# Optimization experiments

Hardware: AMD Instinct MI355X
Metric: run time of the kernel (lower is better)

The kernel has to match this reference:

```python
import jax, jax.numpy as jnp
import numpy as np

N = 20000      # nodes
E = 320000     # edges (every node has >=1 incoming edge)
IN = 512       # input feature dim
HID = 128      # per-head hidden dim
H = 8          # heads
C = 64         # classes (final layer hidden dim)
SLOPE = 0.01   # torch F.leaky_relu default negative_slope


def _gat_head(x, src, dst, W, b, al, alb, ar, arb):
    # x: [N, D_in]; W: [D_in, D_h]; al/ar: [D_h]; alb/arb: scalar
    ft = x @ W + b                       # [N, D_h]
    a1 = ft @ al + alb                   # [N] dst-side logit
    a2 = ft @ ar + arb                   # [N] src-side logit
    s = jax.nn.leaky_relu(a1[dst] + a2[src], SLOPE)   # [E]
    smax = jax.ops.segment_max(s, dst, num_segments=N)
    e = jnp.exp(s - smax[dst])
    denom = jax.ops.segment_sum(e, dst, num_segments=N)
    w = e / denom[dst]                   # segment softmax over incoming edges
    accum = jax.ops.segment_sum(w[:, None] * ft[src], dst, num_segments=N)
    return jax.nn.elu(accum)             # GATFinalize (no residual)


def setup_inputs() -> dict:
    key = jax.random.key(0)
    ks = jax.random.split(key, 16)

    def lin(k, i, o):
        return (jax.random.normal(k, (i, o), jnp.float32) / np.sqrt(i))

    features = jax.random.normal(ks[0], (N, IN), jnp.float32)
    src = jax.random.randint(ks[1], (E,), 0, N, jnp.int32)
    dst = jnp.concatenate([
        jnp.arange(N, dtype=jnp.int32),
        jax.random.randint(ks[2], (E - N,), 0, N, jnp.int32),
    ])

    # layer 0: H heads, in_dim -> HID
    W0 = jax.random.normal(ks[3], (H, IN, HID), jnp.float32) / np.sqrt(IN)
    b0 = jnp.zeros((H, HID), jnp.float32)
    al0 = jax.random.normal(ks[4], (H, HID), jnp.float32) / np.sqrt(HID)
    alb0 = jnp.zeros((H,), jnp.float32)
    ar0 = jax.random.normal(ks[5], (H, HID), jnp.float32) / np.sqrt(HID)
    arb0 = jnp.zeros((H,), jnp.float32)

    # layer 1: H heads, H*HID -> HID
    W1 = jax.random.normal(ks[6], (H, H * HID, HID), jnp.float32) / np.sqrt(H * HID)
    b1 = jnp.zeros((H, HID), jnp.float32)
    al1 = jax.random.normal(ks[7], (H, HID), jnp.float32) / np.sqrt(HID)
    alb1 = jnp.zeros((H,), jnp.float32)
    ar1 = jax.random.normal(ks[8], (H, HID), jnp.float32) / np.sqrt(HID)
    arb1 = jnp.zeros((H,), jnp.float32)

    # final: single head, H*HID -> C
    Wf = lin(ks[9], H * HID, C)
    bf = jnp.zeros((C,), jnp.float32)
    alf = jax.random.normal(ks[10], (C,), jnp.float32) / np.sqrt(C)
    albf = jnp.zeros((), jnp.float32)
    arf = jax.random.normal(ks[11], (C,), jnp.float32) / np.sqrt(C)
    arbf = jnp.zeros((), jnp.float32)

    return dict(features=features, src=src, dst=dst,
                W0=W0, b0=b0, al0=al0, alb0=alb0, ar0=ar0, arb0=arb0,
                W1=W1, b1=b1, al1=al1, alb1=alb1, ar1=ar1, arb1=arb1,
                Wf=Wf, bf=bf, alf=alf, albf=albf, arf=arf, arbf=arbf)


def reference(features, src, dst,
              W0, b0, al0, alb0, ar0, arb0,
              W1, b1, al1, alb1, ar1, arb1,
              Wf, bf, alf, albf, arf, arbf):
    x = features
    # layer 0: concat heads -> [N, H*HID]
    x = jnp.concatenate([
        _gat_head(x, src, dst, W0[h], b0[h], al0[h], alb0[h], ar0[h], arb0[h])
        for h in range(H)], axis=1)
    # layer 1
    x = jnp.concatenate([
        _gat_head(x, src, dst, W1[h], b1[h], al1[h], alb1[h], ar1[h], arb1[h])
        for h in range(H)], axis=1)
    # final single-head output layer -> [N, C]
    return _gat_head(x, src, dst, Wf, bf, alf, albf, arf, arbf)
```

## Files before the change

### kernel.cpp

```cpp
#include <hip/hip_runtime.h>
#include <math.h>

#define N_NODES 20000
#define N_EDGES 320000
#define D_IN    512
#define D_HID   128
#define N_HEADS 8
#define N_CLS   64

typedef __bf16 bf16x8 __attribute__((ext_vector_type(8)));
typedef float  f32x4  __attribute__((ext_vector_type(4)));

__device__ __forceinline__ float leaky(float x) { return fmaxf(x, 0.01f * x); }

__device__ __forceinline__ unsigned short f2bf(float f) {
    unsigned u = __float_as_uint(f);
    return (unsigned short)((u + 0x7FFFu + ((u >> 16) & 1u)) >> 16);
}
__device__ __forceinline__ float bflo(unsigned v) { return __uint_as_float(v << 16); }
__device__ __forceinline__ float bfhi(unsigned v) { return __uint_as_float(v & 0xffff0000u); }

__device__ __forceinline__ void gl_lds16(const void* g, void* l) {
    __builtin_amdgcn_global_load_lds((const __attribute__((address_space(1))) void*)g,
                                     (__attribute__((address_space(3))) void*)l, 16, 0, 0);
}

__global__ void k_zero(int* __restrict__ p, int n) {
    int i = blockIdx.x * blockDim.x + threadIdx.x;
    if (i < n) p[i] = 0;
}

__global__ void k_count(const int* __restrict__ dst, int* __restrict__ counts, int e) {
    int i = blockIdx.x * blockDim.x + threadIdx.x;
    if (i < e) atomicAdd(&counts[dst[i]], 1);
}

__global__ void k_scan(const int* __restrict__ counts, int* __restrict__ indptr,
                       int* __restrict__ cursor, int n) {
    __shared__ int sdata[1024];
    __shared__ int srun;
    int t = threadIdx.x;
    if (t == 0) srun = 0;
    __syncthreads();
    for (int base = 0; base < n; base += 1024) {
        int idx = base + t;
        int v = (idx < n) ? counts[idx] : 0;
        sdata[t] = v;
        __syncthreads();
        for (int off = 1; off < 1024; off <<= 1) {
            int x = (t >= off) ? sdata[t - off] : 0;
            __syncthreads();
            sdata[t] += x;
            __syncthreads();
        }
        int incl = sdata[t];
        int run = srun;
        if (idx < n) {
            indptr[idx] = run + incl - v;
            cursor[idx] = run + incl - v;
        }
        __syncthreads();
        if (t == 1023) srun = run + incl;
        __syncthreads();
    }
    if (t == 0) indptr[n] = srun;
}

__global__ void k_scatter(const int* __restrict__ src, const int* __restrict__ dst,
                          int* __restrict__ cursor, int* __restrict__ csr_src, int e) {
    int i = blockIdx.x * blockDim.x + threadIdx.x;
    if (i < e) {
        int pos = atomicAdd(&cursor[dst[i]], 1);
        csr_src[pos] = src[i];
    }
}

__global__ void k_cvtA(const float* __restrict__ in, unsigned short* __restrict__ out, int n4) {
    int i = blockIdx.x * blockDim.x + threadIdx.x;
    if (i < n4) {
        float4 v = ((const float4*)in)[i];
        unsigned long long pk =
            (unsigned long long)f2bf(v.x) | ((unsigned long long)f2bf(v.y) << 16) |
            ((unsigned long long)f2bf(v.z) << 32) | ((unsigned long long)f2bf(v.w) << 48);
        *(unsigned long long*)(out + (size_t)i * 4) = pk;
    }
}

__global__ void k_cvtW(const float* __restrict__ W, unsigned short* __restrict__ Wt,
                       int K, int Nf) {
    __shared__ float t[64][65];
    int k0 = blockIdx.x * 64, n0 = blockIdx.y * 64, h = blockIdx.z;
    const float* Wh = W + (size_t)h * K * Nf;
    unsigned short* Wth = Wt + (size_t)h * K * Nf;
    int tx = threadIdx.x & 63, ty = threadIdx.x >> 6;
#pragma unroll
    for (int i = 0; i < 16; ++i) {
        int k = ty + i * 4;
        t[k][tx] = Wh[(size_t)(k0 + k) * Nf + n0 + tx];
    }
    __syncthreads();
#pragma unroll
    for (int i = 0; i < 16; ++i) {
        int n = ty + i * 4;
        Wth[(size_t)(n0 + n) * K + k0 + tx] = f2bf(t[tx][n]);
    }
}

__global__ __launch_bounds__(256) void k_gemm_fused(
    const unsigned short* __restrict__ A, const unsigned short* __restrict__ Bt,
    const float* __restrict__ bias, const float* __restrict__ al,
    const float* __restrict__ alb, const float* __restrict__ ar,
    const float* __restrict__ arb, unsigned short* __restrict__ C,
    float* __restrict__ a1, float* __restrict__ a2, int M, int K)
{
    constexpr int BM = 128, BK = 64, BNP = 256;
    __shared__ unsigned short As[BM * BK];
    __shared__ unsigned short Bs[BNP * BK];

    const int tid  = threadIdx.x;
    const int lane = tid & 63;
    const int wid  = tid >> 6;
    const int wm   = wid >> 1;
    const int wn   = wid & 1;
    const int m0   = blockIdx.x * BM;
    const int h0   = blockIdx.z * 2;
    const int h    = h0 + wn;

    const unsigned short* Bth = Bt + (size_t)h0 * 128 * K;
    const int rsub = lane & 15;
    const int rhi  = lane >> 4;
    const int wbase = tid & ~63;

    f32x4 acc[4][8];
#pragma unroll
    for (int i = 0; i < 4; ++i)
#pragma unroll
        for (int j = 0; j < 8; ++j) acc[i][j] = (f32x4){0.f, 0.f, 0.f, 0.f};

    for (int k0 = 0; k0 < K; k0 += BK) {
#pragma unroll
        for (int p = 0; p < 4; ++p) {
            int o    = (p * 256 + tid) * 16;
            int row  = o >> 7;
            int icol = (o & 127) ^ ((row & 7) << 4);
            int grow = m0 + row; if (grow > M - 1) grow = M - 1;
            gl_lds16(A + (size_t)grow * K + k0 + (icol >> 1),
                     (void*)((char*)As + (p * 256 + wbase) * 16));
        }
#pragma unroll
        for (int p = 0; p < 8; ++p) {
            int o    = (p * 256 + tid) * 16;
            int row  = o >> 7;
            int icol = (o & 127) ^ ((row & 7) << 4);
            gl_lds16(Bth + (size_t)row * K + k0 + (icol >> 1),
                     (void*)((char*)Bs + (p * 256 + wbase) * 16));
        }
        __syncthreads();

#pragma unroll
        for (int q = 0; q < 2; ++q) {
            bf16x8 av[4], bv[8];
#pragma unroll
            for (int mi = 0; mi < 4; ++mi) {
                int row  = wm * 64 + mi * 16 + rsub;
                int icol = (q * 64 + rhi * 16) ^ ((row & 7) << 4);
                av[mi] = *(const bf16x8*)((const char*)As + row * 128 + icol);
            }
#pragma unroll
            for (int ni = 0; ni < 8; ++ni) {
                int row  = wn * 128 + ni * 16 + rsub;
                int icol = (q * 64 + rhi * 16) ^ ((row & 7) << 4);
                bv[ni] = *(const bf16x8*)((const char*)Bs + row * 128 + icol);
            }
#pragma unroll
            for (int mi = 0; mi < 4; ++mi)
#pragma unroll
                for (int ni = 0; ni < 8; ++ni)
                    acc[mi][ni] = __builtin_amdgcn_mfma_f32_16x16x32_bf16(
                        av[mi], bv[ni], acc[mi][ni], 0, 0, 0);
        }
        __syncthreads();
    }

#pragma unroll
    for (int ni = 0; ni < 8; ++ni) {
        float bvv = bias[h * 128 + ni * 16 + rsub];
#pragma unroll
        for (int mi = 0; mi < 4; ++mi)
#pragma unroll
            for (int r = 0; r < 4; ++r) acc[mi][ni][r] += bvv;
    }

    unsigned short* Ch = C + (size_t)h * N_NODES * 128;
#pragma unroll
    for (int ni = 0; ni < 8; ++ni) {
        int col = ni * 16 + rsub;
#pragma unroll
        for (int mi = 0; mi < 4; ++mi) {
            int rowb = m0 + wm * 64 + mi * 16 + rhi * 4;
#pragma unroll
            for (int r = 0; r < 4; ++r) {
                int row = rowb + r;
                if (row < M) Ch[(size_t)row * 128 + col] = f2bf(acc[mi][ni][r]);
            }
        }
    }

    float alv[8], arv[8];
#pragma unroll
    for (int ni = 0; ni < 8; ++ni) {
        alv[ni] = al[h * 128 + ni * 16 + rsub];
        arv[ni] = ar[h * 128 + ni * 16 + rsub];
    }
    float albv = alb[h], arbv = arb[h];
#pragma unroll
    for (int mi = 0; mi < 4; ++mi) {
#pragma unroll
        for (int r = 0; r < 4; ++r) {
            float s1 = 0.f, s2 = 0.f;
#pragma unroll
            for (int ni = 0; ni < 8; ++ni) {
                s1 += acc[mi][ni][r] * alv[ni];
                s2 += acc[mi][ni][r] * arv[ni];
            }
#pragma unroll
            for (int off = 1; off <= 8; off <<= 1) {
                s1 += __shfl_xor(s1, off);
                s2 += __shfl_xor(s2, off);
            }
            if (rsub == 0) {
                int row = m0 + wm * 64 + mi * 16 + rhi * 4 + r;
                if (row < M) {
                    a1[row * 8 + h] = s1 + albv;
                    a2[row * 8 + h] = s2 + arbv;
                }
            }
        }
    }
}

template<int BN>
__global__ __launch_bounds__(256) void k_gemm_bf16(
    const unsigned short* __restrict__ A, const unsigned short* __restrict__ Bt,
    const float* __restrict__ bias, unsigned short* __restrict__ C,
    int M, int K, int ldc)
{
    constexpr int BM = 128, BK = 64;
    constexpr int WN    = 1;
    constexpr int MFRAG = 2;
    constexpr int NFRAG = 4;

    __shared__ unsigned short As[BM * BK];
    __shared__ unsigned short Bs[BN * BK];

    const int tid  = threadIdx.x;
    const int lane = tid & 63;
    const int wid  = tid >> 6;
    const int wm   = wid / WN;
    const int wn   = wid % WN;
    const int m0   = blockIdx.x * BM;

    const int rsub = lane & 15;
    const int rhi  = lane >> 4;
    const int wbase = tid & ~63;

    f32x4 acc[MFRAG][NFRAG];
#pragma unroll
    for (int i = 0; i < MFRAG; ++i)
#pragma unroll
        for (int j = 0; j < NFRAG; ++j) acc[i][j] = (f32x4){0.f, 0.f, 0.f, 0.f};

    for (int k0 = 0; k0 < K; k0 += BK) {
#pragma unroll
        for (int p = 0; p < 4; ++p) {
            int o    = (p * 256 + tid) * 16;
            int row  = o >> 7;
            int icol = (o & 127) ^ ((row & 7) << 4);
            int grow = m0 + row; if (grow > M - 1) grow = M - 1;
            gl_lds16(A + (size_t)grow * K + k0 + (icol >> 1),
                     (void*)((char*)As + (p * 256 + wbase) * 16));
        }
#pragma unroll
        for (int p = 0; p < BN / 32; ++p) {
            int o    = (p * 256 + tid) * 16;
            int row  = o >> 7;
            int icol = (o & 127) ^ ((row & 7) << 4);
            gl_lds16(Bt + (size_t)row * K + k0 + (icol >> 1),
                     (void*)((char*)Bs + (p * 256 + wbase) * 16));
        }
        __syncthreads();

        bf16x8 av[2][MFRAG], bv[2][NFRAG];
#pragma unroll
        for (int q = 0; q < 2; ++q) {
#pragma unroll
            for (int mi = 0; mi < MFRAG; ++mi) {
                int row  = wm * (MFRAG * 16) + mi * 16 + rsub;
                int icol = (q * 64 + rhi * 16) ^ ((row & 7) << 4);
                av[q][mi] = *(const bf16x8*)((const char*)As + row * 128 + icol);
            }
#pragma unroll
            for (int ni = 0; ni < NFRAG; ++ni) {
                int row  = wn * (NFRAG * 16) + ni * 16 + rsub;
                int icol = (q * 64 + rhi * 16) ^ ((row & 7) << 4);
                bv[q][ni] = *(const bf16x8*)((const char*)Bs + row * 128 + icol);
            }
        }
#pragma unroll
        for (int q = 0; q < 2; ++q)
#pragma unroll
            for (int mi = 0; mi < MFRAG; ++mi)
#pragma unroll
                for (int ni = 0; ni < NFRAG; ++ni)
                    acc[mi][ni] = __builtin_amdgcn_mfma_f32_16x16x32_bf16(
                        av[q][mi], bv[q][ni], acc[mi][ni], 0, 0, 0);
        __syncthreads();
    }

#pragma unroll
    for (int ni = 0; ni < NFRAG; ++ni) {
        int col  = wn * (NFRAG * 16) + ni * 16 + rsub;
        float bvv = bias[col];
#pragma unroll
        for (int mi = 0; mi < MFRAG; ++mi) {
            int rowb = m0 + wm * (MFRAG * 16) + mi * 16 + rhi * 4;
#pragma unroll
            for (int r = 0; r < 4; ++r) {
                int row = rowb + r;
                if (row < M) C[(size_t)row * ldc + col] = f2bf(acc[mi][ni][r] + bvv);
            }
        }
    }
}

__global__ __launch_bounds__(256) void k_alogit(
    const unsigned short* __restrict__ ft, const float* __restrict__ al,
    const float* __restrict__ alb, const float* __restrict__ ar,
    const float* __restrict__ arb, float* __restrict__ a1,
    float* __restrict__ a2, int H_, int Dh)
{
    int n = blockIdx.x * 4 + (threadIdx.x >> 6);
    int lane = threadIdx.x & 63;
    if (n >= N_NODES) return;
    for (int h = 0; h < H_; ++h) {
        size_t base = ((size_t)h * N_NODES + n) * Dh;
        float s1 = 0.f, s2 = 0.f;
        for (int j0 = 2 * lane; j0 < Dh; j0 += 128) {
            unsigned v = *(const unsigned*)(ft + base + j0);
            float lo = bflo(v), hi = bfhi(v);
            float2 A = *(const float2*)(al + h * Dh + j0);
            float2 R = *(const float2*)(ar + h * Dh + j0);
            s1 += lo * A.x + hi * A.y;
            s2 += lo * R.x + hi * R.y;
        }
#pragma unroll
        for (int off = 32; off > 0; off >>= 1) {
            s1 += __shfl_xor(s1, off);
            s2 += __shfl_xor(s2, off);
        }
        if (lane == 0) {
            a1[n * H_ + h] = s1 + alb[h];
            a2[n * H_ + h] = s2 + arb[h];
        }
    }
}

__global__ __launch_bounds__(256) void k_aggregate8(
    const unsigned short* __restrict__ ft, const float* __restrict__ a1,
    const float* __restrict__ a2, const int* __restrict__ indptr,
    const int* __restrict__ csr_src, unsigned short* __restrict__ outp)
{
    int h = blockIdx.x & 7;
    int n = (blockIdx.x >> 3) * 4 + (threadIdx.x >> 6);
    int lane = threadIdx.x & 63;
    if (n >= N_NODES) return;
    const unsigned short* fth = ft + (size_t)h * N_NODES * 128;
    size_t obase = (size_t)n * 1024 + h * 128;
    int start = indptr[n], end = indptr[n + 1];
    int q   = lane & 15;
    int sub = lane >> 4;

    if (end <= start) {
        if (lane < 16) { uint4 z = make_uint4(0, 0, 0, 0); *(uint4*)(outp + obase + 8 * q) = z; }
        return;
    }
    float a1v = a1[n * 8 + h];

    int sidx0 = 0; float sv0 = 0.f;
    float m = -INFINITY;
    {
        int e = start + lane;
        if (e < end) {
            sidx0 = csr_src[e];
            sv0 = leaky(a1v + a2[sidx0 * 8 + h]);
            m = sv0;
        }
        for (int e2 = start + 64 + lane; e2 < end; e2 += 64)
            m = fmaxf(m, leaky(a1v + a2[csr_src[e2] * 8 + h]));
#pragma unroll
        for (int off = 32; off > 0; off >>= 1) m = fmaxf(m, __shfl_xor(m, off));
    }

    float denom = 0.f;
    float4 accA = make_float4(0.f, 0.f, 0.f, 0.f);
    float4 accB = make_float4(0.f, 0.f, 0.f, 0.f);
    for (int base = start; base < end; base += 64) {
        int ee = base + lane;
        float wgt = 0.f;
        int sidx = sidx0;
        if (base == start) {
            if (ee < end) wgt = expf(sv0 - m);
        } else if (ee < end) {
            sidx = csr_src[ee];
            wgt = expf(leaky(a1v + a2[sidx * 8 + h]) - m);
        }
        denom += wgt;
        int cnt = min(64, end - base);

        auto iss = [&](int i, float& W, int& S, uint4& V) {
            int j  = i + sub;
            int jc = (j < cnt) ? j : (cnt - 1);
            W = __shfl(wgt, jc);
            S = __shfl(sidx, jc);
            if (j >= cnt) W = 0.f;
            V = *(const uint4*)(fth + (size_t)S * 128 + 8 * q);
        };
        auto accf = [&](const uint4& V, float W) {
            accA.x += W * bflo(V.x); accA.y += W * bfhi(V.x);
            accA.z += W * bflo(V.y); accA.w += W * bfhi(V.y);
            accB.x += W * bflo(V.z); accB.y += W * bfhi(V.z);
            accB.z += W * bflo(V.w); accB.w += W * bfhi(V.w);
        };

        int i = 0;
        for (; i + 16 <= cnt; i += 16) {
            float w0, w1, w2, w3; int s0, s1, s2, s3; uint4 v0, v1, v2, v3;
            iss(i, w0, s0, v0); iss(i + 4, w1, s1, v1);
            iss(i + 8, w2, s2, v2); iss(i + 12, w3, s3, v3);
            accf(v0, w0); accf(v1, w1); accf(v2, w2); accf(v3, w3);
        }
        for (; i < cnt; i += 8) {
            float w0, w1; int s0, s1; uint4 v0, v1;
            iss(i, w0, s0, v0); iss(i + 4, w1, s1, v1);
            accf(v0, w0); accf(v1, w1);
        }
    }
#pragma unroll
    for (int off = 32; off > 0; off >>= 1) denom += __shfl_xor(denom, off);
#pragma unroll
    for (int off = 16; off <= 32; off <<= 1) {
        accA.x += __shfl_xor(accA.x, off); accA.y += __shfl_xor(accA.y, off);
        accA.z += __shfl_xor(accA.z, off); accA.w += __shfl_xor(accA.w, off);
        accB.x += __shfl_xor(accB.x, off); accB.y += __shfl_xor(accB.y, off);
        accB.z += __shfl_xor(accB.z, off); accB.w += __shfl_xor(accB.w, off);
    }
    float inv = 1.f / denom;
    if (lane < 16) {
        float r[8] = {accA.x * inv, accA.y * inv, accA.z * inv, accA.w * inv,
                      accB.x * inv, accB.y * inv, accB.z * inv, accB.w * inv};
        unsigned pk[4];
#pragma unroll
        for (int u = 0; u < 4; ++u) {
            float e0 = (r[2*u]   > 0.f) ? r[2*u]   : expm1f(r[2*u]);
            float e1 = (r[2*u+1] > 0.f) ? r[2*u+1] : expm1f(r[2*u+1]);
            pk[u] = (unsigned)f2bf(e0) | ((unsigned)f2bf(e1) << 16);
        }
        *(uint4*)(outp + obase + 8 * q) = make_uint4(pk[0], pk[1], pk[2], pk[3]);
    }
}

__global__ __launch_bounds__(256) void k_aggregate_final(
    const unsigned short* __restrict__ ft, const float* __restrict__ a1,
    const float* __restrict__ a2, const int* __restrict__ indptr,
    const int* __restrict__ csr_src, float* __restrict__ outp)
{
    int n = blockIdx.x * 4 + (threadIdx.x >> 6);
    int lane = threadIdx.x & 63;
    if (n >= N_NODES) return;
    size_t obase = (size_t)n * 64;
    int start = indptr[n], end = indptr[n + 1];

    if (end <= start) {
        if (lane < 32) *(float2*)(outp + obase + 2 * lane) = make_float2(0.f, 0.f);
        return;
    }
    float a1v = a1[n];

    int sidx0 = 0; float sv0 = 0.f;
    float m = -INFINITY;
    {
        int e = start + lane;
        if (e < end) {
            sidx0 = csr_src[e];
            sv0 = leaky(a1v + a2[sidx0]);
            m = sv0;
        }
        for (int e2 = start + 64 + lane; e2 < end; e2 += 64)
            m = fmaxf(m, leaky(a1v + a2[csr_src[e2]]));
#pragma unroll
        for (int off = 32; off > 0; off >>= 1) m = fmaxf(m, __shfl_xor(m, off));
    }

    float denom = 0.f, acc0 = 0.f, acc1 = 0.f;
    int half = lane >> 5, idx = lane & 31;
    for (int base = start; base < end; base += 64) {
        int e = base + lane;
        float wgt = 0.f;
        int sidx = sidx0;
        if (base == start) {
            if (e < end) wgt = expf(sv0 - m);
        } else if (e < end) {
            sidx = csr_src[e];
            wgt = expf(leaky(a1v + a2[sidx]) - m);
        }
        denom += wgt;
        int cnt = min(64, end - base);
        for (int i = 0; i < cnt; i += 4) {
            int j0 = i + half, j1 = i + 2 + half;
            int jc0 = (j0 < cnt) ? j0 : (cnt - 1);
            int jc1 = (j1 < cnt) ? j1 : (cnt - 1);
            float w0 = __shfl(wgt, jc0); int s0 = __shfl(sidx, jc0);
            float w1 = __shfl(wgt, jc1); int s1 = __shfl(sidx, jc1);
            if (j0 >= cnt) w0 = 0.f;
            if (j1 >= cnt) w1 = 0.f;
            unsigned v0 = *(const unsigned*)(ft + (size_t)s0 * 64 + 2 * idx);
            unsigned v1 = *(const unsigned*)(ft + (size_t)s1 * 64 + 2 * idx);
            acc0 += w0 * bflo(v0) + w1 * bflo(v1);
            acc1 += w0 * bfhi(v0) + w1 * bfhi(v1);
        }
    }
#pragma unroll
    for (int off = 32; off > 0; off >>= 1) denom += __shfl_xor(denom, off);
    float inv = 1.f / denom;

    acc0 += __shfl_xor(acc0, 32);
    acc1 += __shfl_xor(acc1, 32);
    float r0 = acc0 * inv, r1 = acc1 * inv;
    r0 = (r0 > 0.f) ? r0 : expm1f(r0);
    r1 = (r1 > 0.f) ? r1 : expm1f(r1);
    if (lane < 32)
        *(float2*)(outp + obase + 2 * lane) = make_float2(r0, r1);
}

extern "C" void kernel_launch(void* const* d_in, const int* in_sizes, int n_in,
                              void* d_out, int out_size, void* d_ws, size_t ws_size,
                              hipStream_t stream) {
    const float* features = (const float*)d_in[0];
    const int*   src      = (const int*)d_in[1];
    const int*   dst      = (const int*)d_in[2];
    const float* W0  = (const float*)d_in[3];
    const float* b0  = (const float*)d_in[4];
    const float* al0 = (const float*)d_in[5];
    const float* alb0= (const float*)d_in[6];
    const float* ar0 = (const float*)d_in[7];
    const float* arb0= (const float*)d_in[8];
    const float* W1  = (const float*)d_in[9];
    const float* b1  = (const float*)d_in[10];
    const float* al1 = (const float*)d_in[11];
    const float* alb1= (const float*)d_in[12];
    const float* ar1 = (const float*)d_in[13];
    const float* arb1= (const float*)d_in[14];
    const float* Wf  = (const float*)d_in[15];
    const float* bff = (const float*)d_in[16];
    const float* alf = (const float*)d_in[17];
    const float* albf= (const float*)d_in[18];
    const float* arf = (const float*)d_in[19];
    const float* arbf= (const float*)d_in[20];
    float* out = (float*)d_out;

    char* wp = (char*)d_ws;
    unsigned short* ft16  = (unsigned short*)wp;  wp += (size_t)N_NODES * 1024 * 2;
    unsigned short* xb16  = (unsigned short*)wp;  wp += (size_t)N_NODES * 1024 * 2;
    unsigned short* feat16= (unsigned short*)wp;  wp += (size_t)N_NODES * 512 * 2;
    unsigned short* w0t   = (unsigned short*)wp;  wp += (size_t)N_HEADS * D_HID * D_IN * 2;
    unsigned short* w1t   = (unsigned short*)wp;  wp += (size_t)N_HEADS * D_HID * 1024 * 2;
    unsigned short* wft   = (unsigned short*)wp;  wp += (size_t)N_CLS * 1024 * 2;
    float* a1             = (float*)wp;           wp += (size_t)N_NODES * N_HEADS * 4;
    float* a2             = (float*)wp;           wp += (size_t)N_NODES * N_HEADS * 4;
    int* counts = (int*)wp;                       wp += (size_t)N_NODES * 4;
    int* indptr = (int*)wp;                       wp += (size_t)(N_NODES + 1) * 4;
    int* cursor = (int*)wp;                       wp += (size_t)N_NODES * 4;
    int* csr    = (int*)wp;

    k_zero<<<(N_NODES + 255) / 256, 256, 0, stream>>>(counts, N_NODES);
    k_count<<<(N_EDGES + 255) / 256, 256, 0, stream>>>(dst, counts, N_EDGES);
    k_scan<<<1, 1024, 0, stream>>>(counts, indptr, cursor, N_NODES);
    k_scatter<<<(N_EDGES + 255) / 256, 256, 0, stream>>>(src, dst, cursor, csr, N_EDGES);

    k_cvtA<<<(N_NODES * D_IN / 4 + 255) / 256, 256, 0, stream>>>(features, feat16, N_NODES * D_IN / 4);
    k_cvtW<<<dim3(D_IN / 64, D_HID / 64, N_HEADS), 256, 0, stream>>>(W0, w0t, D_IN, D_HID);
    k_cvtW<<<dim3(1024 / 64, D_HID / 64, N_HEADS), 256, 0, stream>>>(W1, w1t, 1024, D_HID);
    k_cvtW<<<dim3(1024 / 64, N_CLS / 64, 1), 256, 0, stream>>>(Wf, wft, 1024, N_CLS);

    const int gm = (N_NODES + 127) / 128;
    int nodeBlocks = (N_NODES + 3) / 4;
    int aggBlocksH = 8 * nodeBlocks;

    k_gemm_fused<<<dim3(gm, 1, N_HEADS / 2), 256, 0, stream>>>(
        feat16, w0t, b0, al0, alb0, ar0, arb0, ft16, a1, a2, N_NODES, D_IN);
    k_aggregate8<<<aggBlocksH, 256, 0, stream>>>(ft16, a1, a2, indptr, csr, xb16);

    k_gemm_fused<<<dim3(gm, 1, N_HEADS / 2), 256, 0, stream>>>(
        xb16, w1t, b1, al1, alb1, ar1, arb1, ft16, a1, a2, N_NODES, 1024);
    k_aggregate8<<<aggBlocksH, 256, 0, stream>>>(ft16, a1, a2, indptr, csr, xb16);

    k_gemm_bf16<64><<<dim3(gm, 1, 1), 256, 0, stream>>>(
        xb16, wft, bff, ft16, N_NODES, 1024, N_CLS);
    k_alogit<<<nodeBlocks, 256, 0, stream>>>(ft16, alf, albf, arf, arbf, a1, a2, 1, N_CLS);
    k_aggregate_final<<<nodeBlocks, 256, 0, stream>>>(ft16, a1, a2, indptr, csr, out);
}
```

Before: 646.3 us.

## Store head features node-major and aggregate all heads per wave

The fused GEMM now writes per-head features interleaved as [node][head*128] rather than head-major. The aggregation kernel has one wave process all 8 heads of a node. It computes the max and softmax weights for 8 heads at once from vectorized a1/a2 loads, stages weights and source indices in LDS, and gathers full 2KB source rows with contiguous 16-byte loads. This replaces 8 separate per-head passes over the edge list and index/logit reads, in exchange for more registers and LDS traffic per wave.

```diff
diff --git a/kernel.cpp b/kernel.cpp
--- a/kernel.cpp
+++ b/kernel.cpp
@@ -191,17 +191,16 @@
             for (int r = 0; r < 4; ++r) acc[mi][ni][r] += bvv;
     }
 
-    unsigned short* Ch = C + (size_t)h * N_NODES * 128;
 #pragma unroll
     for (int ni = 0; ni < 8; ++ni) {
-        int col = ni * 16 + rsub;
+        int col = h * 128 + ni * 16 + rsub;
 #pragma unroll
         for (int mi = 0; mi < 4; ++mi) {
             int rowb = m0 + wm * 64 + mi * 16 + rhi * 4;
 #pragma unroll
             for (int r = 0; r < 4; ++r) {
                 int row = rowb + r;
-                if (row < M) Ch[(size_t)row * 128 + col] = f2bf(acc[mi][ni][r]);
+                if (row < M) C[(size_t)row * 1024 + col] = f2bf(acc[mi][ni][r]);
             }
         }
     }
@@ -365,108 +364,176 @@
     }
 }
 
-__global__ __launch_bounds__(256) void k_aggregate8(
+__global__ __launch_bounds__(256) void k_aggregate_ah(
     const unsigned short* __restrict__ ft, const float* __restrict__ a1,
     const float* __restrict__ a2, const int* __restrict__ indptr,
     const int* __restrict__ csr_src, unsigned short* __restrict__ outp)
 {
-    int h = blockIdx.x & 7;
-    int n = (blockIdx.x >> 3) * 4 + (threadIdx.x >> 6);
-    int lane = threadIdx.x & 63;
+    __shared__ float wtab[2][4][64][8];
+    __shared__ int   stab[2][4][64];
+
+    const int wid  = threadIdx.x >> 6;
+    const int lane = threadIdx.x & 63;
+    int n = blockIdx.x * 4 + wid;
     if (n >= N_NODES) return;
-    const unsigned short* fth = ft + (size_t)h * N_NODES * 128;
-    size_t obase = (size_t)n * 1024 + h * 128;
     int start = indptr[n], end = indptr[n + 1];
-    int q   = lane & 15;
-    int sub = lane >> 4;
+    unsigned short* op = outp + (size_t)n * 1024;
 
     if (end <= start) {
-        if (lane < 16) { uint4 z = make_uint4(0, 0, 0, 0); *(uint4*)(outp + obase + 8 * q) = z; }
+        uint4 z = make_uint4(0, 0, 0, 0);
+        *(uint4*)(op + lane * 8) = z;
+        *(uint4*)(op + 512 + lane * 8) = z;
         return;
     }
-    float a1v = a1[n * 8 + h];
-
-    int sidx0 = 0; float sv0 = 0.f;
-    float m = -INFINITY;
+
+    float a1v[8];
+    *(float4*)&a1v[0] = *(const float4*)(a1 + n * 8);
+    *(float4*)&a1v[4] = *(const float4*)(a1 + n * 8 + 4);
+
+    float m[8], sv0[8];
+    int sidx0 = 0;
+#pragma unroll
+    for (int h = 0; h < 8; ++h) { m[h] = -INFINITY; sv0[h] = -INFINITY; }
     {
         int e = start + lane;
         if (e < end) {
             sidx0 = csr_src[e];
-            sv0 = leaky(a1v + a2[sidx0 * 8 + h]);
-            m = sv0;
-        }
-        for (int e2 = start + 64 + lane; e2 < end; e2 += 64)
-            m = fmaxf(m, leaky(a1v + a2[csr_src[e2] * 8 + h]));
-#pragma unroll
-        for (int off = 32; off > 0; off >>= 1) m = fmaxf(m, __shfl_xor(m, off));
-    }
-
-    float denom = 0.f;
-    float4 accA = make_float4(0.f, 0.f, 0.f, 0.f);
-    float4 accB = make_float4(0.f, 0.f, 0.f, 0.f);
-    for (int base = start; base < end; base += 64) {
-        int ee = base + lane;
-        float wgt = 0.f;
-        int sidx = sidx0;
+            float4 x0 = *(const float4*)(a2 + (size_t)sidx0 * 8);
+            float4 x1 = *(const float4*)(a2 + (size_t)sidx0 * 8 + 4);
+            sv0[0] = leaky(a1v[0] + x0.x); sv0[1] = leaky(a1v[1] + x0.y);
+            sv0[2] = leaky(a1v[2] + x0.z); sv0[3] = leaky(a1v[3] + x0.w);
+            sv0[4] = leaky(a1v[4] + x1.x); sv0[5] = leaky(a1v[5] + x1.y);
+            sv0[6] = leaky(a1v[6] + x1.z); sv0[7] = leaky(a1v[7] + x1.w);
+#pragma unroll
+            for (int h = 0; h < 8; ++h) m[h] = sv0[h];
+        }
+        for (int e2 = start + 64 + lane; e2 < end; e2 += 64) {
+            int s = csr_src[e2];
+            float4 x0 = *(const float4*)(a2 + (size_t)s * 8);
+            float4 x1 = *(const float4*)(a2 + (size_t)s * 8 + 4);
+            m[0] = fmaxf(m[0], leaky(a1v[0] + x0.x)); m[1] = fmaxf(m[1], leaky(a1v[1] + x0.y));
+            m[2] = fmaxf(m[2], leaky(a1v[2] + x0.z)); m[3] = fmaxf(m[3], leaky(a1v[3] + x0.w));
+            m[4] = fmaxf(m[4], leaky(a1v[4] + x1.x)); m[5] = fmaxf(m[5], leaky(a1v[5] + x1.y));
+            m[6] = fmaxf(m[6], leaky(a1v[6] + x1.z)); m[7] = fmaxf(m[7], leaky(a1v[7] + x1.w));
+        }
+#pragma unroll
+        for (int h = 0; h < 8; ++h)
+#pragma unroll
+            for (int off = 32; off > 0; off >>= 1)
+                m[h] = fmaxf(m[h], __shfl_xor(m[h], off));
+    }
+
+    float denom[8];
+    float acc[16];
+#pragma unroll
+    for (int h = 0; h < 8; ++h) denom[h] = 0.f;
+#pragma unroll
+    for (int i = 0; i < 16; ++i) acc[i] = 0.f;
+
+    int pb = 0;
+    for (int base = start; base < end; base += 64, pb ^= 1) {
+        int e = base + lane;
+        int cnt = min(64, end - base);
+        float w[8];
+        int sidx = 0;
         if (base == start) {
-            if (ee < end) wgt = expf(sv0 - m);
-        } else if (ee < end) {
-            sidx = csr_src[ee];
-            wgt = expf(leaky(a1v + a2[sidx * 8 + h]) - m);
-        }
-        denom += wgt;
-        int cnt = min(64, end - base);
-
-        auto iss = [&](int i, float& W, int& S, uint4& V) {
-            int j  = i + sub;
-            int jc = (j < cnt) ? j : (cnt - 1);
-            W = __shfl(wgt, jc);
-            S = __shfl(sidx, jc);
-            if (j >= cnt) W = 0.f;
-            V = *(const uint4*)(fth + (size_t)S * 128 + 8 * q);
-        };
-        auto accf = [&](const uint4& V, float W) {
-            accA.x += W * bflo(V.x); accA.y += W * bfhi(V.x);
-            accA.z += W * bflo(V.y); accA.w += W * bfhi(V.y);
-            accB.x += W * bflo(V.z); accB.y += W * bfhi(V.z);
-            accB.z += W * bflo(V.w); accB.w += W * bfhi(V.w);
-        };
-
-        int i = 0;
-        for (; i + 16 <= cnt; i += 16) {
-            float w0, w1, w2, w3; int s0, s1, s2, s3; uint4 v0, v1, v2, v3;
-            iss(i, w0, s0, v0); iss(i + 4, w1, s1, v1);
-            iss(i + 8, w2, s2, v2); iss(i + 12, w3, s3, v3);
-            accf(v0, w0); accf(v1, w1); accf(v2, w2); accf(v3, w3);
-        }
-        for (; i < cnt; i += 8) {
-            float w0, w1; int s0, s1; uint4 v0, v1;
-            iss(i, w0, s0, v0); iss(i + 4, w1, s1, v1);
-            accf(v0, w0); accf(v1, w1);
-        }
-    }
-#pragma unroll
-    for (int off = 32; off > 0; off >>= 1) denom += __shfl_xor(denom, off);
-#pragma unroll
-    for (int off = 16; off <= 32; off <<= 1) {
-        accA.x += __shfl_xor(accA.x, off); accA.y += __shfl_xor(accA.y, off);
-        accA.z += __shfl_xor(accA.z, off); accA.w += __shfl_xor(accA.w, off);
-        accB.x += __shfl_xor(accB.x, off); accB.y += __shfl_xor(accB.y, off);
-        accB.z += __shfl_xor(accB.z, off); accB.w += __shfl_xor(accB.w, off);
-    }
-    float inv = 1.f / denom;
-    if (lane < 16) {
-        float r[8] = {accA.x * inv, accA.y * inv, accA.z * inv, accA.w * inv,
-                      accB.x * inv, accB.y * inv, accB.z * inv, accB.w * inv};
-        unsigned pk[4];
-#pragma unroll
-        for (int u = 0; u < 4; ++u) {
-            float e0 = (r[2*u]   > 0.f) ? r[2*u]   : expm1f(r[2*u]);
-            float e1 = (r[2*u+1] > 0.f) ? r[2*u+1] : expm1f(r[2*u+1]);
-            pk[u] = (unsigned)f2bf(e0) | ((unsigned)f2bf(e1) << 16);
-        }
-        *(uint4*)(outp + obase + 8 * q) = make_uint4(pk[0], pk[1], pk[2], pk[3]);
-    }
+            sidx = sidx0;
+            if (e < end) {
+#pragma unroll
+                for (int h = 0; h < 8; ++h) w[h] = expf(sv0[h] - m[h]);
+            } else {
+#pragma unroll
+                for (int h = 0; h < 8; ++h) w[h] = 0.f;
+            }
+        } else if (e < end) {
+            sidx = csr_src[e];
+            float4 x0 = *(const float4*)(a2 + (size_t)sidx * 8);
+            float4 x1 = *(const float4*)(a2 + (size_t)sidx * 8 + 4);
+            w[0] = expf(leaky(a1v[0] + x0.x) - m[0]); w[1] = expf(leaky(a1v[1] + x0.y) - m[1]);
+            w[2] = expf(leaky(a1v[2] + x0.z) - m[2]); w[3] = expf(leaky(a1v[3] + x0.w) - m[3]);
+            w[4] = expf(leaky(a1v[4] + x1.x) - m[4]); w[5] = expf(leaky(a1v[5] + x1.y) - m[5]);
+            w[6] = expf(leaky(a1v[6] + x1.z) - m[6]); w[7] = expf(leaky(a1v[7] + x1.w) - m[7]);
+        } else {
+#pragma unroll
+            for (int h = 0; h < 8; ++h) w[h] = 0.f;
+        }
+#pragma unroll
+        for (int h = 0; h < 8; ++h) denom[h] += w[h];
+
+        *(float4*)&wtab[pb][wid][lane][0] = *(float4*)&w[0];
+        *(float4*)&wtab[pb][wid][lane][4] = *(float4*)&w[4];
+        stab[pb][wid][lane] = sidx;
+        asm volatile("s_waitcnt lgkmcnt(0)" ::: "memory");
+
+        const float* wrow = &wtab[pb][wid][0][0];
+        const int*   srow = &stab[pb][wid][0];
+        const int myh = lane >> 4;
+        for (int j = 0; j < cnt; j += 2) {
+            int j1ok = (j + 1 < cnt);
+            int j1 = j1ok ? j + 1 : j;
+            int s0 = srow[j];
+            int s1 = srow[j1];
+            float w00 = wrow[j * 8 + myh];
+            float w01 = wrow[j * 8 + 4 + myh];
+            float w10 = j1ok ? wrow[j1 * 8 + myh] : 0.f;
+            float w11 = j1ok ? wrow[j1 * 8 + 4 + myh] : 0.f;
+            const unsigned short* f0 = ft + (size_t)s0 * 1024;
+            const unsigned short* f1 = ft + (size_t)s1 * 1024;
+            uint4 v00 = *(const uint4*)(f0 + lane * 8);
+            uint4 v01 = *(const uint4*)(f0 + 512 + lane * 8);
+            uint4 v10 = *(const uint4*)(f1 + lane * 8);
+            uint4 v11 = *(const uint4*)(f1 + 512 + lane * 8);
+            acc[0]  += w00 * bflo(v00.x); acc[1]  += w00 * bfhi(v00.x);
+            acc[2]  += w00 * bflo(v00.y); acc[3]  += w00 * bfhi(v00.y);
+            acc[4]  += w00 * bflo(v00.z); acc[5]  += w00 * bfhi(v00.z);
+            acc[6]  += w00 * bflo(v00.w); acc[7]  += w00 * bfhi(v00.w);
+            acc[8]  += w01 * bflo(v01.x); acc[9]  += w01 * bfhi(v01.x);
+            acc[10] += w01 * bflo(v01.y); acc[11] += w01 * bfhi(v01.y);
+            acc[12] += w01 * bflo(v01.z); acc[13] += w01 * bfhi(v01.z);
+            acc[14] += w01 * bflo(v01.w); acc[15] += w01 * bfhi(v01.w);
+            acc[0]  += w10 * bflo(v10.x); acc[1]  += w10 * bfhi(v10.x);
+            acc[2]  += w10 * bflo(v10.y); acc[3]  += w10 * bfhi(v10.y);
+            acc[4]  += w10 * bflo(v10.z); acc[5]  += w10 * bfhi(v10.z);
+            acc[6]  += w10 * bflo(v10.w); acc[7]  += w10 * bfhi(v10.w);
+            acc[8]  += w11 * bflo(v11.x); acc[9]  += w11 * bfhi(v11.x);
+            acc[10] += w11 * bflo(v11.y); acc[11] += w11 * bfhi(v11.y);
+            acc[12] += w11 * bflo(v11.z); acc[13] += w11 * bfhi(v11.z);
+            acc[14] += w11 * bflo(v11.w); acc[15] += w11 * bfhi(v11.w);
+        }
+    }
+
+#pragma unroll
+    for (int h = 0; h < 8; ++h)
+#pragma unroll
+        for (int off = 32; off > 0; off >>= 1)
+            denom[h] += __shfl_xor(denom[h], off);
+
+    float t01 = (lane & 16) ? denom[1] : denom[0];
+    float t23 = (lane & 16) ? denom[3] : denom[2];
+    float dlo = (lane & 32) ? t23 : t01;
+    float t45 = (lane & 16) ? denom[5] : denom[4];
+    float t67 = (lane & 16) ? denom[7] : denom[6];
+    float dhi = (lane & 32) ? t67 : t45;
+    float inv0 = 1.f / dlo;
+    float inv1 = 1.f / dhi;
+
+    unsigned pk[4];
+#pragma unroll
+    for (int u = 0; u < 4; ++u) {
+        float r0 = acc[2 * u] * inv0, r1 = acc[2 * u + 1] * inv0;
+        r0 = (r0 > 0.f) ? r0 : expm1f(r0);
+        r1 = (r1 > 0.f) ? r1 : expm1f(r1);
+        pk[u] = (unsigned)f2bf(r0) | ((unsigned)f2bf(r1) << 16);
+    }
+    *(uint4*)(op + lane * 8) = make_uint4(pk[0], pk[1], pk[2], pk[3]);
+#pragma unroll
+    for (int u = 0; u < 4; ++u) {
+        float r0 = acc[8 + 2 * u] * inv1, r1 = acc[8 + 2 * u + 1] * inv1;
+        r0 = (r0 > 0.f) ? r0 : expm1f(r0);
+        r1 = (r1 > 0.f) ? r1 : expm1f(r1);
+        pk[u] = (unsigned)f2bf(r0) | ((unsigned)f2bf(r1) << 16);
+    }
+    *(uint4*)(op + 512 + lane * 8) = make_uint4(pk[0], pk[1], pk[2], pk[3]);
 }
 
 __global__ __launch_bounds__(256) void k_aggregate_final(
@@ -594,15 +661,14 @@
 
     const int gm = (N_NODES + 127) / 128;
     int nodeBlocks = (N_NODES + 3) / 4;
-    int aggBlocksH = 8 * nodeBlocks;
 
     k_gemm_fused<<<dim3(gm, 1, N_HEADS / 2), 256, 0, stream>>>(
         feat16, w0t, b0, al0, alb0, ar0, arb0, ft16, a1, a2, N_NODES, D_IN);
-    k_aggregate8<<<aggBlocksH, 256, 0, stream>>>(ft16, a1, a2, indptr, csr, xb16);
+    k_aggregate_ah<<<nodeBlocks, 256, 0, stream>>>(ft16, a1, a2, indptr, csr, xb16);
 
     k_gemm_fused<<<dim3(gm, 1, N_HEADS / 2), 256, 0, stream>>>(
         xb16, w1t, b1, al1, alb1, ar1, arb1, ft16, a1, a2, N_NODES, 1024);
-    k_aggregate8<<<aggBlocksH, 256, 0, stream>>>(ft16, a1, a2, indptr, csr, xb16);
+    k_aggregate_ah<<<nodeBlocks, 256, 0, stream>>>(ft16, a1, a2, indptr, csr, xb16);
 
     k_gemm_bf16<64><<<dim3(gm, 1, 1), 256, 0, stream>>>(
         xb16, wft, bff, ft16, N_NODES, 1024, N_CLS);
```

New measurement: 616.7 us. 1.05x faster.
